# Kernel tuning notes

Hardware: AMD Instinct MI355X
Metric: run time of the kernel (lower is better)

Reference implementation:

```python
import jax, jax.numpy as jnp
import numpy as np

N_CTX = 4096
D_MODEL = 2048
D_HEAD = 128


def setup_inputs() -> dict:
    key = jax.random.key(0)
    k1, k2, k3, k4 = jax.random.split(key, 4)
    x = jax.random.normal(k1, (N_CTX, D_MODEL), dtype=jnp.float32)
    # torch nn.Linear weights are [out, in]; kept in that layout.
    Wk = jax.random.normal(k2, (D_HEAD, D_MODEL), dtype=jnp.float32) * (1.0 / np.sqrt(D_MODEL))
    Wq = jax.random.normal(k3, (D_HEAD, D_MODEL), dtype=jnp.float32) * (1.0 / np.sqrt(D_MODEL))
    W2 = jax.random.normal(k4, (D_MODEL, D_MODEL), dtype=jnp.float32) * (1.0 / np.sqrt(D_MODEL))
    return {"x": x, "Wk": Wk, "Wq": Wq, "W2": W2}


def reference(x, Wk, Wq, W2):
    # Faithful to the torch module: no 1/sqrt(d_head) scaling, V = x itself.
    n = x.shape[0]
    q = x @ Wq.T                     # [n, d_head]
    k = x @ Wk.T                     # [n, d_head]
    scores = q @ k.T                 # [n, n]
    # causal mask: strictly-upper-triangular entries -> -inf
    causal = jnp.tril(jnp.ones((n, n), dtype=bool))
    scores = jnp.where(causal, scores, -jnp.inf)
    attn = jax.nn.softmax(scores, axis=1)  # [n, n]
    out = attn @ x                   # [n, d_model] (V is the raw input)
    return out @ W2.T                # [n, d_model]
```

## Files before the change

### kernel.cpp

```cpp
#include <hip/hip_runtime.h>

#define NCTX 4096
#define DMODEL 2048
#define DHEAD 128

typedef _Float16 f16;
typedef f16 f16x8 __attribute__((ext_vector_type(8)));
typedef float f32x4 __attribute__((ext_vector_type(4)));
typedef unsigned short u16;
typedef u16 u16x8 __attribute__((ext_vector_type(8)));

__device__ __forceinline__ u16 f2h(float f) {
  union { f16 h; u16 u; } v; v.h = (f16)f; return v.u;
}
__device__ __forceinline__ float h2f(u16 u) {
  union { u16 u; f16 h; } v; v.u = u; return (float)v.h;
}

__device__ __forceinline__ void gl_lds16(const void* g, void* l) {
  __builtin_amdgcn_global_load_lds((const __attribute__((address_space(1))) void*)g,
                                   (__attribute__((address_space(3))) void*)l, 16, 0, 0);
}

__device__ __forceinline__ void splitH4(float4 v, ushort4& h, ushort4& l) {
  h.x = f2h(v.x); l.x = f2h(v.x - h2f(h.x));
  h.y = f2h(v.y); l.y = f2h(v.y - h2f(h.y));
  h.z = f2h(v.z); l.z = f2h(v.z - h2f(h.z));
  h.w = f2h(v.w); l.w = f2h(v.w - h2f(h.w));
}

__global__ __launch_bounds__(256) void prep_all(const float* __restrict__ x,
                                                const float* __restrict__ Wq,
                                                const float* __restrict__ Wk,
                                                const float* __restrict__ W2,
                                                u16* __restrict__ xh, u16* __restrict__ xl,
                                                u16* __restrict__ Wf, u16* __restrict__ W2f,
                                                u16* __restrict__ XT) {
  __shared__ float tile[64][65];
  int b = blockIdx.x;
  int t = threadIdx.x;
  if (b < 2048) {
    int mb = (b >> 5) * 64, db = (b & 31) * 64;
    int tx = t & 15, ty = t >> 4;
#pragma unroll
    for (int rr = 0; rr < 4; ++rr) {
      int row = rr * 16 + ty;
      float4 v = *(const float4*)(x + (size_t)(mb + row) * DMODEL + db + tx * 4);
      ushort4 h, l; splitH4(v, h, l);
      size_t gi = ((size_t)(mb + row) * DMODEL + db) / 4 + tx;
      ((ushort4*)xh)[gi] = h; ((ushort4*)xl)[gi] = l;
      tile[row][tx * 4 + 0] = v.x; tile[row][tx * 4 + 1] = v.y;
      tile[row][tx * 4 + 2] = v.z; tile[row][tx * 4 + 3] = v.w;
    }
    __syncthreads();
#pragma unroll
    for (int rr = 0; rr < 4; ++rr) {
      int r = (t >> 4) * 4 + rr;
      int c0 = (t & 15) * 4;
      ushort4 o;
      o.x = f2h(tile[c0 + 0][r]); o.y = f2h(tile[c0 + 1][r]);
      o.z = f2h(tile[c0 + 2][r]); o.w = f2h(tile[c0 + 3][r]);
      *(ushort4*)(XT + (size_t)(db + r) * NCTX + mb + c0) = o;
    }
  } else if (b < 2560) {
    int wk = (b >= 2304);
    int i = (b - (wk ? 2304 : 2048)) * 256 + t;
    const float* W = wk ? Wk : Wq;
    size_t off = wk ? ((size_t)DHEAD * DMODEL / 4) : 0;
    float4 v = ((const float4*)W)[i];
    ushort4 o;
    o.x = f2h(v.x); o.y = f2h(v.y); o.z = f2h(v.z); o.w = f2h(v.w);
    ((ushort4*)Wf)[off + i] = o;
  } else {
    int i = (b - 2560) * 256 + t;
    float4 v = ((const float4*)W2)[i];
    ushort4 o;
    o.x = f2h(v.x); o.y = f2h(v.y); o.z = f2h(v.z); o.w = f2h(v.w);
    ((ushort4*)W2f)[i] = o;
  }
}

__global__ __launch_bounds__(256) void reduce8_f16(const float* __restrict__ P,
                                                   u16* __restrict__ out, int n4) {
  int i = blockIdx.x * 256 + threadIdx.x;
  if (i >= n4) return;
  float4 s = ((const float4*)P)[i];
#pragma unroll
  for (int z = 1; z < 8; ++z) {
    float4 v = ((const float4*)P)[(size_t)z * n4 + i];
    s.x += v.x; s.y += v.y; s.z += v.z; s.w += v.w;
  }
  ushort4 o;
  o.x = f2h(s.x); o.y = f2h(s.y); o.z = f2h(s.z); o.w = f2h(s.w);
  ((ushort4*)out)[i] = o;
}

__global__ __launch_bounds__(256) void reduce_c4(const u16* __restrict__ P,
                                                 u16* __restrict__ out, size_t cs) {
  int row = blockIdx.x;
  int t = threadIdx.x;
  int nc = (row >> 10) + 1;
  size_t base = (size_t)row * DMODEL + t * 8;
  float s[8] = {};
  for (int c = 0; c < nc; ++c) {
    u16x8 v = *(const u16x8*)(P + (size_t)c * cs + base);
#pragma unroll
    for (int k = 0; k < 8; ++k) s[k] += h2f(v[k]);
  }
  u16x8 o;
#pragma unroll
  for (int k = 0; k < 8; ++k) o[k] = f2h(s[k]);
  *(u16x8*)(out + base) = o;
}

__global__ __launch_bounds__(256) void reduce2_hf(const u16* __restrict__ P0,
                                                  const u16* __restrict__ P1,
                                                  float* __restrict__ out, int n8) {
  int i = blockIdx.x * 256 + threadIdx.x;
  if (i >= n8) return;
  u16x8 a = ((const u16x8*)P0)[i];
  u16x8 b = ((const u16x8*)P1)[i];
  float4 o0, o1;
  o0.x = h2f(a[0]) + h2f(b[0]); o0.y = h2f(a[1]) + h2f(b[1]);
  o0.z = h2f(a[2]) + h2f(b[2]); o0.w = h2f(a[3]) + h2f(b[3]);
  o1.x = h2f(a[4]) + h2f(b[4]); o1.y = h2f(a[5]) + h2f(b[5]);
  o1.z = h2f(a[6]) + h2f(b[6]); o1.w = h2f(a[7]) + h2f(b[7]);
  ((float4*)out)[i * 2 + 0] = o0;
  ((float4*)out)[i * 2 + 1] = o1;
}

__global__ __launch_bounds__(256) void softmax_rows(const float* __restrict__ S,
                                                    u16* __restrict__ P) {
  int i = blockIdx.x;
  int t = threadIdx.x;
  __shared__ float rowbuf[NCTX];
  __shared__ float red[4];
  __shared__ float red2[4];
  const float* srow = S + (size_t)i * NCTX;
  int len = i + 1;
  int jmax = ((i >> 7) + 1) << 7;
  float mx = -3.0e38f;
  for (int j = t * 4; j < len; j += 1024) {
    if (j + 4 <= len) {
      float4 v = *(const float4*)(srow + j);
      *(float4*)(rowbuf + j) = v;
      mx = fmaxf(mx, fmaxf(fmaxf(v.x, v.y), fmaxf(v.z, v.w)));
    } else {
      for (int k = j; k < len; ++k) {
        float v = srow[k];
        rowbuf[k] = v;
        mx = fmaxf(mx, v);
      }
    }
  }
#pragma unroll
  for (int o = 32; o > 0; o >>= 1) mx = fmaxf(mx, __shfl_xor(mx, o, 64));
  if ((t & 63) == 0) red[t >> 6] = mx;
  __syncthreads();
  mx = fmaxf(fmaxf(red[0], red[1]), fmaxf(red[2], red[3]));
  float sum = 0.f;
  for (int j = t; j < len; j += 256) {
    float e = __expf(rowbuf[j] - mx);
    rowbuf[j] = e;
    sum += e;
  }
#pragma unroll
  for (int o = 32; o > 0; o >>= 1) sum += __shfl_xor(sum, o, 64);
  if ((t & 63) == 0) red2[t >> 6] = sum;
  __syncthreads();
  float inv = 1.0f / (red2[0] + red2[1] + red2[2] + red2[3]);
  u16* prow = P + (size_t)i * NCTX;
  for (int j = t * 4; j < jmax; j += 1024) {
    ushort4 o;
    o.x = (j + 0 < len) ? f2h(rowbuf[j + 0] * inv) : (u16)0;
    o.y = (j + 1 < len) ? f2h(rowbuf[j + 1] * inv) : (u16)0;
    o.z = (j + 2 < len) ? f2h(rowbuf[j + 2] * inv) : (u16)0;
    o.w = (j + 3 < len) ? f2h(rowbuf[j + 3] * inv) : (u16)0;
    *(ushort4*)(prow + j) = o;
  }
}

__global__ __launch_bounds__(256, 4) void gemm_f16_p(const u16* __restrict__ A,
                                                     const u16* __restrict__ B,
                                                     float* __restrict__ C,
                                                     int lda, int ldb, int ldc,
                                                     int K, int KC, size_t chunkStride,
                                                     int causal, int tri) {
  int bm = gridDim.x - 1 - blockIdx.x, bn = blockIdx.y, kc = blockIdx.z;
  if (tri && bn > bm) return;
  int kEnd = K;
  if (causal) { int ke = (bm + 1) * 128; if (ke < kEnd) kEnd = ke; }
  int kStart = kc * KC;
  if (kStart >= kEnd) return;
  int kStop = kStart + KC < kEnd ? kStart + KC : kEnd;
  __shared__ __align__(16) u16 As[128 * 64];
  __shared__ __align__(16) u16 Bs[128 * 64];
  int t = threadIdx.x;
  int lane = t & 63, w = t >> 6;
  int m0 = bm * 128, n0 = bn * 128;
  int wm = (w >> 1) * 64, wn = (w & 1) * 64;
  int mfrag = lane & 15, quad = lane >> 4;
  int srow = t >> 3, schunk = t & 7;
  int rsw = mfrag & 7;
  f32x4 acc[4][4] = {};
  for (int kt = kStart; kt < kStop; kt += 64) {
#pragma unroll
    for (int p = 0; p < 4; ++p) {
      int row = p * 32 + srow;
      int gsc = schunk ^ (row & 7);
      gl_lds16(A + (size_t)(m0 + row) * lda + kt + gsc * 8, As + (size_t)(p * 256 + t) * 8);
      gl_lds16(B + (size_t)(n0 + row) * ldb + kt + gsc * 8, Bs + (size_t)(p * 256 + t) * 8);
    }
    __syncthreads();
#pragma unroll
    for (int ks = 0; ks < 2; ++ks) {
      int c0 = ((ks * 4 + quad) ^ rsw) * 8;
      f16x8 af[4], bfr[4];
#pragma unroll
      for (int i = 0; i < 4; ++i)
        af[i] = *(const f16x8*)(As + (wm + i * 16 + mfrag) * 64 + c0);
#pragma unroll
      for (int j = 0; j < 4; ++j)
        bfr[j] = *(const f16x8*)(Bs + (wn + j * 16 + mfrag) * 64 + c0);
#pragma unroll
      for (int i = 0; i < 4; ++i)
#pragma unroll
        for (int j = 0; j < 4; ++j)
          acc[i][j] = __builtin_amdgcn_mfma_f32_16x16x32_f16(af[i], bfr[j], acc[i][j], 0, 0, 0);
    }
    __syncthreads();
  }
  float* Cc = C + (size_t)kc * chunkStride;
#pragma unroll
  for (int i = 0; i < 4; ++i)
#pragma unroll
    for (int j = 0; j < 4; ++j)
#pragma unroll
      for (int rr = 0; rr < 4; ++rr) {
        int row = m0 + wm + i * 16 + quad * 4 + rr;
        int col = n0 + wn + j * 16 + mfrag;
        Cc[(size_t)row * ldc + col] = acc[i][j][rr];
      }
}

__global__ __launch_bounds__(256, 4) void gemm_f16_h(const u16* __restrict__ A,
                                                     const u16* __restrict__ B,
                                                     u16* __restrict__ C,
                                                     int lda, int ldb, int ldc,
                                                     int K, int KC, size_t chunkStride,
                                                     int causal) {
  int bm = gridDim.x - 1 - blockIdx.x, bn = blockIdx.y, kc = blockIdx.z;
  int kEnd = K;
  if (causal) { int ke = (bm + 1) * 128; if (ke < kEnd) kEnd = ke; }
  int kStart = kc * KC;
  if (kStart >= kEnd) return;
  int kStop = kStart + KC < kEnd ? kStart + KC : kEnd;
  __shared__ __align__(16) u16 As[128 * 64];
  __shared__ __align__(16) u16 Bs[128 * 64];
  int t = threadIdx.x;
  int lane = t & 63, w = t >> 6;
  int m0 = bm * 128, n0 = bn * 128;
  int wm = (w >> 1) * 64, wn = (w & 1) * 64;
  int mfrag = lane & 15, quad = lane >> 4;
  int srow = t >> 3, schunk = t & 7;
  int rsw = mfrag & 7;
  f32x4 acc[4][4] = {};
  for (int kt = kStart; kt < kStop; kt += 64) {
#pragma unroll
    for (int p = 0; p < 4; ++p) {
      int row = p * 32 + srow;
      int gsc = schunk ^ (row & 7);
      gl_lds16(A + (size_t)(m0 + row) * lda + kt + gsc * 8, As + (size_t)(p * 256 + t) * 8);
      gl_lds16(B + (size_t)(n0 + row) * ldb + kt + gsc * 8, Bs + (size_t)(p * 256 + t) * 8);
    }
    __syncthreads();
#pragma unroll
    for (int ks = 0; ks < 2; ++ks) {
      int c0 = ((ks * 4 + quad) ^ rsw) * 8;
      f16x8 af[4], bfr[4];
#pragma unroll
      for (int i = 0; i < 4; ++i)
        af[i] = *(const f16x8*)(As + (wm + i * 16 + mfrag) * 64 + c0);
#pragma unroll
      for (int j = 0; j < 4; ++j)
        bfr[j] = *(const f16x8*)(Bs + (wn + j * 16 + mfrag) * 64 + c0);
#pragma unroll
      for (int i = 0; i < 4; ++i)
#pragma unroll
        for (int j = 0; j < 4; ++j)
          acc[i][j] = __builtin_amdgcn_mfma_f32_16x16x32_f16(af[i], bfr[j], acc[i][j], 0, 0, 0);
    }
    __syncthreads();
  }
  u16* Cc = C + (size_t)kc * chunkStride;
#pragma unroll
  for (int i = 0; i < 4; ++i)
#pragma unroll
    for (int j = 0; j < 4; ++j)
#pragma unroll
      for (int rr = 0; rr < 4; ++rr) {
        int row = m0 + wm + i * 16 + quad * 4 + rr;
        int col = n0 + wn + j * 16 + mfrag;
        Cc[(size_t)row * ldc + col] = f2h(acc[i][j][rr]);
      }
}

__global__ __launch_bounds__(256, 3) void gemm_f16x2_p(const u16* __restrict__ Ah,
                                                       const u16* __restrict__ Al,
                                                       const u16* __restrict__ B,
                                                       float* __restrict__ C,
                                                       int lda, int ldb, int ldc,
                                                       int K, int KC, size_t chunkStride) {
  int bm = blockIdx.x, bn = blockIdx.y, kc = blockIdx.z;
  int kStart = kc * KC;
  int kStop = kStart + KC < K ? kStart + KC : K;
  __shared__ __align__(16) u16 Ash[128 * 64];
  __shared__ __align__(16) u16 Asl[128 * 64];
  __shared__ __align__(16) u16 Bs[128 * 64];
  int t = threadIdx.x;
  int lane = t & 63, w = t >> 6;
  int m0 = bm * 128, n0 = bn * 128;
  int wm = (w >> 1) * 64, wn = (w & 1) * 64;
  int mfrag = lane & 15, quad = lane >> 4;
  int srow = t >> 3, schunk = t & 7;
  int rsw = mfrag & 7;
  f32x4 acc[4][4] = {};
  for (int kt = kStart; kt < kStop; kt += 64) {
#pragma unroll
    for (int p = 0; p < 4; ++p) {
      int row = p * 32 + srow;
      int gsc = schunk ^ (row & 7);
      size_t aoff = (size_t)(m0 + row) * lda + kt + gsc * 8;
      size_t loff = (size_t)(p * 256 + t) * 8;
      gl_lds16(Ah + aoff, Ash + loff);
      gl_lds16(Al + aoff, Asl + loff);
      gl_lds16(B + (size_t)(n0 + row) * ldb + kt + gsc * 8, Bs + loff);
    }
    __syncthreads();
#pragma unroll
    for (int ks = 0; ks < 2; ++ks) {
      int c0 = ((ks * 4 + quad) ^ rsw) * 8;
      f16x8 a0[4], bfr[4];
#pragma unroll
      for (int j = 0; j < 4; ++j)
        bfr[j] = *(const f16x8*)(Bs + (wn + j * 16 + mfrag) * 64 + c0);
#pragma unroll
      for (int i = 0; i < 4; ++i)
        a0[i] = *(const f16x8*)(Ash + (wm + i * 16 + mfrag) * 64 + c0);
#pragma unroll
      for (int i = 0; i < 4; ++i)
#pragma unroll
        for (int j = 0; j < 4; ++j)
          acc[i][j] = __builtin_amdgcn_mfma_f32_16x16x32_f16(a0[i], bfr[j], acc[i][j], 0, 0, 0);
#pragma unroll
      for (int i = 0; i < 4; ++i)
        a0[i] = *(const f16x8*)(Asl + (wm + i * 16 + mfrag) * 64 + c0);
#pragma unroll
      for (int i = 0; i < 4; ++i)
#pragma unroll
        for (int j = 0; j < 4; ++j)
          acc[i][j] = __builtin_amdgcn_mfma_f32_16x16x32_f16(a0[i], bfr[j], acc[i][j], 0, 0, 0);
    }
    __syncthreads();
  }
  float* Cc = C + (size_t)kc * chunkStride;
#pragma unroll
  for (int i = 0; i < 4; ++i)
#pragma unroll
    for (int j = 0; j < 4; ++j)
#pragma unroll
      for (int rr = 0; rr < 4; ++rr) {
        int row = m0 + wm + i * 16 + quad * 4 + rr;
        int col = n0 + wn + j * 16 + mfrag;
        Cc[(size_t)row * ldc + col] = acc[i][j][rr];
      }
}

extern "C" void kernel_launch(void* const* d_in, const int* in_sizes, int n_in,
                              void* d_out, int out_size, void* d_ws, size_t ws_size,
                              hipStream_t stream) {
  const float* x  = (const float*)d_in[0];
  const float* Wk = (const float*)d_in[1];
  const float* Wq = (const float*)d_in[2];
  const float* W2 = (const float*)d_in[3];

  char* ws = (char*)d_ws;
  const size_t MB = 1024 * 1024;
  u16*   QKf  = (u16*)  (ws + 0);
  u16*   Wf   = (u16*)  (ws + 2 * MB);
  u16*   xT   = (u16*)  (ws + 3 * MB);
  u16*   W2f  = (u16*)  (ws + 19 * MB);
  u16*   outb = (u16*)  (ws + 27 * MB);
  u16*   attn = (u16*)  (ws + 43 * MB);
  u16*   xh   = (u16*)  (ws + 75 * MB);
  u16*   xl   = (u16*)  (ws + 91 * MB);
  float* QKp  = (float*)(ws + 107 * MB);
  float* S    = (float*)(ws + 75 * MB);
  u16*   Ph   = (u16*)  (ws + 75 * MB);

  const int XN8 = NCTX * DMODEL / 8;
  const int QKN4 = NCTX * 256 / 4;
  const size_t CS = (size_t)NCTX * DMODEL;

  prep_all<<<6656, 256, 0, stream>>>(x, Wq, Wk, W2, xh, xl, Wf, W2f, xT);

  gemm_f16x2_p<<<dim3(NCTX / 128, 2, 8), 256, 0, stream>>>(
      xh, xl, Wf, QKp, DMODEL, DMODEL, 256, DMODEL, 256, (size_t)NCTX * 256);
  reduce8_f16<<<(QKN4 + 255) / 256, 256, 0, stream>>>(QKp, QKf, QKN4);

  gemm_f16_p<<<dim3(NCTX / 128, NCTX / 128, 1), 256, 0, stream>>>(
      QKf, QKf + DHEAD, S, 256, 256, NCTX, DHEAD, DHEAD, 0, 0, 1);
  softmax_rows<<<NCTX, 256, 0, stream>>>(S, attn);

  gemm_f16_h<<<dim3(NCTX / 128, DMODEL / 128, 4), 256, 0, stream>>>(
      attn, xT, Ph, NCTX, NCTX, DMODEL, NCTX, 1024, CS, 1);
  reduce_c4<<<NCTX, 256, 0, stream>>>(Ph, outb, CS);

  gemm_f16_h<<<dim3(NCTX / 128, DMODEL / 128, 2), 256, 0, stream>>>(
      outb, W2f, Ph, DMODEL, DMODEL, DMODEL, DMODEL, 1024, CS, 0);
  reduce2_hf<<<(XN8 + 255) / 256, 256, 0, stream>>>(Ph, Ph + CS, (float*)d_out, XN8);
}
```

Measured before the change: 271.4 us.

## Cut split-K partials: direct-write unsplit causal blocks, single-pass final GEMM

The attn@x GEMM now uses a split-K of 2 with chunk 2048. Blocks whose whole causal K range fits in one chunk (the first 2048 rows) write straight to the final buffer, so only the lower half of rows needs the two-way partial reduction. The final projection GEMM drops split-K and writes fp32 output directly through gemm_f16_p, which removes the reduce2_hf pass and its partial-buffer traffic. In exchange the projection GEMM runs with less grid parallelism (512 blocks), and the causal GEMM has more load imbalance across its chunks.

```diff
diff --git a/kernel.cpp b/kernel.cpp
--- a/kernel.cpp
+++ b/kernel.cpp
@@ -95,38 +95,17 @@
   ((ushort4*)out)[i] = o;
 }
 
-__global__ __launch_bounds__(256) void reduce_c4(const u16* __restrict__ P,
+__global__ __launch_bounds__(256) void reduce_c2(const u16* __restrict__ P,
                                                  u16* __restrict__ out, size_t cs) {
-  int row = blockIdx.x;
-  int t = threadIdx.x;
-  int nc = (row >> 10) + 1;
+  int row = 2048 + blockIdx.x;
+  int t = threadIdx.x;
   size_t base = (size_t)row * DMODEL + t * 8;
-  float s[8] = {};
-  for (int c = 0; c < nc; ++c) {
-    u16x8 v = *(const u16x8*)(P + (size_t)c * cs + base);
-#pragma unroll
-    for (int k = 0; k < 8; ++k) s[k] += h2f(v[k]);
-  }
+  u16x8 a = *(const u16x8*)(P + base);
+  u16x8 b = *(const u16x8*)(P + cs + base);
   u16x8 o;
 #pragma unroll
-  for (int k = 0; k < 8; ++k) o[k] = f2h(s[k]);
+  for (int k = 0; k < 8; ++k) o[k] = f2h(h2f(a[k]) + h2f(b[k]));
   *(u16x8*)(out + base) = o;
-}
-
-__global__ __launch_bounds__(256) void reduce2_hf(const u16* __restrict__ P0,
-                                                  const u16* __restrict__ P1,
-                                                  float* __restrict__ out, int n8) {
-  int i = blockIdx.x * 256 + threadIdx.x;
-  if (i >= n8) return;
-  u16x8 a = ((const u16x8*)P0)[i];
-  u16x8 b = ((const u16x8*)P1)[i];
-  float4 o0, o1;
-  o0.x = h2f(a[0]) + h2f(b[0]); o0.y = h2f(a[1]) + h2f(b[1]);
-  o0.z = h2f(a[2]) + h2f(b[2]); o0.w = h2f(a[3]) + h2f(b[3]);
-  o1.x = h2f(a[4]) + h2f(b[4]); o1.y = h2f(a[5]) + h2f(b[5]);
-  o1.z = h2f(a[6]) + h2f(b[6]); o1.w = h2f(a[7]) + h2f(b[7]);
-  ((float4*)out)[i * 2 + 0] = o0;
-  ((float4*)out)[i * 2 + 1] = o1;
 }
 
 __global__ __launch_bounds__(256) void softmax_rows(const float* __restrict__ S,
@@ -246,6 +225,7 @@
 __global__ __launch_bounds__(256, 4) void gemm_f16_h(const u16* __restrict__ A,
                                                      const u16* __restrict__ B,
                                                      u16* __restrict__ C,
+                                                     u16* __restrict__ Cf,
                                                      int lda, int ldb, int ldc,
                                                      int K, int KC, size_t chunkStride,
                                                      int causal) {
@@ -292,7 +272,7 @@
     }
     __syncthreads();
   }
-  u16* Cc = C + (size_t)kc * chunkStride;
+  u16* Cc = (kStart == 0 && kStop == kEnd) ? Cf : (C + (size_t)kc * chunkStride);
 #pragma unroll
   for (int i = 0; i < 4; ++i)
 #pragma unroll
@@ -398,7 +378,6 @@
   float* S    = (float*)(ws + 75 * MB);
   u16*   Ph   = (u16*)  (ws + 75 * MB);
 
-  const int XN8 = NCTX * DMODEL / 8;
   const int QKN4 = NCTX * 256 / 4;
   const size_t CS = (size_t)NCTX * DMODEL;
 
@@ -412,11 +391,10 @@
       QKf, QKf + DHEAD, S, 256, 256, NCTX, DHEAD, DHEAD, 0, 0, 1);
   softmax_rows<<<NCTX, 256, 0, stream>>>(S, attn);
 
-  gemm_f16_h<<<dim3(NCTX / 128, DMODEL / 128, 4), 256, 0, stream>>>(
-      attn, xT, Ph, NCTX, NCTX, DMODEL, NCTX, 1024, CS, 1);
-  reduce_c4<<<NCTX, 256, 0, stream>>>(Ph, outb, CS);
-
   gemm_f16_h<<<dim3(NCTX / 128, DMODEL / 128, 2), 256, 0, stream>>>(
-      outb, W2f, Ph, DMODEL, DMODEL, DMODEL, DMODEL, 1024, CS, 0);
-  reduce2_hf<<<(XN8 + 255) / 256, 256, 0, stream>>>(Ph, Ph + CS, (float*)d_out, XN8);
-}
+      attn, xT, Ph, outb, NCTX, NCTX, DMODEL, NCTX, 2048, CS, 1);
+  reduce_c2<<<2048, 256, 0, stream>>>(Ph, outb, CS);
+
+  gemm_f16_p<<<dim3(NCTX / 128, DMODEL / 128, 1), 256, 0, stream>>>(
+      outb, W2f, (float*)d_out, DMODEL, DMODEL, DMODEL, DMODEL, DMODEL, 0, 0, 0);
+}
```

After: 256.8 us. -5.4%, faster.
